# Kernel optimization log

Hardware: AMD Instinct MI355X
Metric: run time of the kernel (lower is better)

The kernel has to match this reference:

```python
import jax, jax.numpy as jnp
import numpy as np

NUM_EMBEDDINGS = 512
EMBEDDING_DIM = 64
COMMITMENT_COST = 0.25


def setup_inputs() -> dict:
    key = jax.random.key(0)
    k1, k2 = jax.random.split(key)
    inputs = jax.random.normal(k1, (64, 32, 32, EMBEDDING_DIM), dtype=jnp.float32)
    # nn.Embedding weight init: uniform(-1/K, 1/K)
    codebook = jax.random.uniform(
        k2, (NUM_EMBEDDINGS, EMBEDDING_DIM), dtype=jnp.float32,
        minval=-1.0 / NUM_EMBEDDINGS, maxval=1.0 / NUM_EMBEDDINGS)
    return {"inputs": inputs, "codebook": codebook}


def reference(inputs, codebook):
    D = codebook.shape[1]
    K = codebook.shape[0]
    flat = inputs.reshape(-1, D)  # [N, D]
    # Squared euclidean distances (argmin-equivalent to torch.cdist output)
    d2 = (jnp.sum(flat * flat, axis=1, keepdims=True)
          - 2.0 * (flat @ codebook.T)
          + jnp.sum(codebook * codebook, axis=1))  # [N, K]
    idx = jnp.argmin(d2, axis=1)  # [N]
    # Gather codebook rows (== one-hot @ codebook in the original)
    quantized = codebook[idx].reshape(inputs.shape)
    e_latent_loss = jnp.mean((jax.lax.stop_gradient(quantized) - inputs) ** 2)
    q_latent_loss = jnp.mean((quantized - jax.lax.stop_gradient(inputs)) ** 2)
    loss = q_latent_loss + COMMITMENT_COST * e_latent_loss
    # Straight-through estimator
    quantized_st = inputs + jax.lax.stop_gradient(quantized - inputs)
    # Perplexity from code usage histogram (== mean of one-hot encodings)
    n = flat.shape[0]
    avg_probs = jnp.zeros((K,), dtype=jnp.float32).at[idx].add(1.0) / n
    perplexity = jnp.exp(-jnp.sum(avg_probs * jnp.log(avg_probs + 1e-10)))
    encoding_indices = idx[:, None]  # [N, 1] to match torch unsqueeze(1)
    return (loss, quantized_st, perplexity, encoding_indices)
```

## Files before the change

kernel.cpp:

```cpp
#include <hip/hip_runtime.h>
#include <math.h>

#define K_EMB 512
#define DIM 64
#define NVEC 65536
#define OUT_LOSS 0
#define OUT_Q 1
#define OUT_PERP (1 + NVEC * DIM)
#define OUT_IDX (1 + NVEC * DIM + 1)
#define EPS2 1e-4f
#define FIX_CAP 16

typedef __attribute__((ext_vector_type(8))) short short8;
typedef __attribute__((ext_vector_type(4))) float float4v;


__device__ __forceinline__ unsigned short bf16_rn(float f) {
    unsigned u = __float_as_uint(f);
    return (unsigned short)((u + 0x7FFFu + ((u >> 16) & 1u)) >> 16);
}

__device__ __forceinline__ float np_pairwise8_sq(const float* v) {
    float r[8];
#pragma unroll
    for (int j = 0; j < 8; ++j) r[j] = __fmul_rn(v[j], v[j]);
#pragma unroll
    for (int i = 8; i < 64; i += 8) {
#pragma unroll
        for (int j = 0; j < 8; ++j) r[j] = __fadd_rn(r[j], __fmul_rn(v[i + j], v[i + j]));
    }
    return __fadd_rn(__fadd_rn(__fadd_rn(r[0], r[1]), __fadd_rn(r[2], r[3])),
                     __fadd_rn(__fadd_rn(r[4], r[5]), __fadd_rn(r[6], r[7])));
}

__global__ void vq_frag(const float* __restrict__ codebook, float* __restrict__ csq,
                        unsigned short* __restrict__ ahi, unsigned short* __restrict__ alo,
                        float4* __restrict__ csqf, unsigned* __restrict__ hist,
                        double* __restrict__ sse64) {
    const int tid = threadIdx.x;
    if (blockIdx.x < 16) {
        const int id = blockIdx.x * 256 + tid;
        const int t = id >> 7, step = (id >> 6) & 1, lane = id & 63;
        const int m = t * 16 + (lane & 15);
        const int kb = step * 32 + (lane >> 4) * 8;
        const float4* src = (const float4*)(codebook + (m << 6) + kb);
        float4 f0 = src[0], f1 = src[1];
        const float fs[8] = {f0.x, f0.y, f0.z, f0.w, f1.x, f1.y, f1.z, f1.w};
        short8 h, l;
#pragma unroll
        for (int j = 0; j < 8; ++j) {
            unsigned short hv = bf16_rn(fs[j]);
            float lof = fs[j] - __uint_as_float(((unsigned)hv) << 16);
            h[j] = (short)hv;
            l[j] = (short)bf16_rn(lof);
        }
        const int fo = ((t * 2 + step) * 64 + lane) * 8;
        *(short8*)(ahi + fo) = h;
        *(short8*)(alo + fo) = l;
    } else {
        __shared__ float s_csq[512];
#pragma unroll
        for (int r = 0; r < 2; ++r) {
            const int k = tid + 256 * r;
            float v = np_pairwise8_sq(codebook + ((size_t)k << 6));
            s_csq[k] = v;
            csq[k] = v;
            hist[k] = 0u;
        }
        if (tid < 64) sse64[tid] = 0.0;
        __syncthreads();
#pragma unroll
        for (int i = 0; i < 8; ++i) {
            const int id = i * 256 + tid;
            const int t = id >> 6, lane = id & 63;
            const int k0 = t * 16 + (lane >> 4) * 4;
            csqf[id] = make_float4(s_csq[k0], s_csq[k0 + 1], s_csq[k0 + 2], s_csq[k0 + 3]);
        }
    }
}

__launch_bounds__(256, 4)
__global__ void vq_main(const float* __restrict__ inputs, const float* __restrict__ codebook,
                        const float* __restrict__ csq, const unsigned short* __restrict__ ahi,
                        const unsigned short* __restrict__ alo, const float4* __restrict__ csqf,
                        unsigned* __restrict__ hist, double* __restrict__ sse64,
                        float* __restrict__ out) {
    __shared__ __align__(16) float s_x[32 * 68];
    __shared__ float s_A[32];
    __shared__ unsigned long long s_t1[4][32];
    __shared__ unsigned long long s_t2[4][32];
    __shared__ unsigned long long s_e[32];
    __shared__ int s_fix[FIX_CAP];
    __shared__ int s_nfix;
    __shared__ float s_w[4];

    const int tid = threadIdx.x;
    const int wave = tid >> 6, lane = tid & 63;
    const int vbase = blockIdx.x * 32;

    if (tid == 0) s_nfix = 0;

    {
        const float4* src = (const float4*)(inputs + ((size_t)vbase << 6));
#pragma unroll
        for (int i = 0; i < 2; ++i) {
            const int f = i * 256 + tid;
            float4 v = src[f];
            *(float4*)&s_x[(f >> 4) * 68 + (f & 15) * 4] = v;
        }
    }
    __syncthreads();

    if (tid < 32) s_A[tid] = np_pairwise8_sq(&s_x[tid * 68]);
    __syncthreads();

    short8 bhi[2][2], blo[2][2];
#pragma unroll
    for (int vt = 0; vt < 2; ++vt) {
        const int vrow = vt * 16 + (lane & 15);
#pragma unroll
        for (int step = 0; step < 2; ++step) {
            const int kb = step * 32 + (lane >> 4) * 8;
            float4 f0 = *(const float4*)&s_x[vrow * 68 + kb];
            float4 f1 = *(const float4*)&s_x[vrow * 68 + kb + 4];
            const float fs[8] = {f0.x, f0.y, f0.z, f0.w, f1.x, f1.y, f1.z, f1.w};
            short8 h, l;
#pragma unroll
            for (int j = 0; j < 8; ++j) {
                unsigned short hv = bf16_rn(fs[j]);
                float lof = fs[j] - __uint_as_float(((unsigned)hv) << 16);
                h[j] = (short)hv;
                l[j] = (short)bf16_rn(lof);
            }
            bhi[vt][step] = h;
            blo[vt][step] = l;
        }
    }

    unsigned long long e1[2] = {~0ULL, ~0ULL}, e2[2] = {~0ULL, ~0ULL};

#pragma unroll 2
    for (int tt = 0; tt < 8; ++tt) {
        const int t = wave * 8 + tt;
        const int fo0 = ((t * 2 + 0) * 64 + lane) * 8;
        const int fo1 = ((t * 2 + 1) * 64 + lane) * 8;
        short8 ah0 = *(const short8*)(ahi + fo0);
        short8 ah1 = *(const short8*)(ahi + fo1);
        short8 al0 = *(const short8*)(alo + fo0);
        short8 al1 = *(const short8*)(alo + fo1);
        float4 cs = csqf[t * 64 + lane];
        const float csr[4] = {cs.x, cs.y, cs.z, cs.w};
#pragma unroll
        for (int vt = 0; vt < 2; ++vt) {
            float4v acc = {0.f, 0.f, 0.f, 0.f};
            acc = __builtin_amdgcn_mfma_f32_16x16x32_bf16(ah0, bhi[vt][0], acc, 0, 0, 0);
            acc = __builtin_amdgcn_mfma_f32_16x16x32_bf16(ah1, bhi[vt][1], acc, 0, 0, 0);
            acc = __builtin_amdgcn_mfma_f32_16x16x32_bf16(ah0, blo[vt][0], acc, 0, 0, 0);
            acc = __builtin_amdgcn_mfma_f32_16x16x32_bf16(ah1, blo[vt][1], acc, 0, 0, 0);
            acc = __builtin_amdgcn_mfma_f32_16x16x32_bf16(al0, bhi[vt][0], acc, 0, 0, 0);
            acc = __builtin_amdgcn_mfma_f32_16x16x32_bf16(al1, bhi[vt][1], acc, 0, 0, 0);
            const float Avt = s_A[vt * 16 + (lane & 15)];
#pragma unroll
            for (int r = 0; r < 4; ++r) {
                float d2 = __fadd_rn(__fsub_rn(Avt, __fmul_rn(2.0f, acc[r])), csr[r]);
                const unsigned k = (unsigned)(t * 16 + (lane >> 4) * 4 + r);
                unsigned long long e = ((unsigned long long)__float_as_uint(d2) << 32) | k;
                if (e < e1[vt]) { e2[vt] = e1[vt]; e1[vt] = e; }
                else if (e < e2[vt]) e2[vt] = e;
            }
        }
    }

#pragma unroll
    for (int vt = 0; vt < 2; ++vt) {
#pragma unroll
        for (int off = 16; off <= 32; off <<= 1) {
            unsigned long long o1 = __shfl_xor(e1[vt], off);
            unsigned long long o2 = __shfl_xor(e2[vt], off);
            if (o1 < e1[vt]) { e2[vt] = (e1[vt] < o2) ? e1[vt] : o2; e1[vt] = o1; }
            else if (o1 < e2[vt]) e2[vt] = o1;
        }
        if (lane < 16) {
            s_t1[wave][vt * 16 + lane] = e1[vt];
            s_t2[wave][vt * 16 + lane] = e2[vt];
        }
    }
    __syncthreads();

    if (tid < 32) {
        unsigned long long E1 = ~0ULL, E2 = ~0ULL;
#pragma unroll
        for (int w = 0; w < 4; ++w) {
            unsigned long long a = s_t1[w][tid], b = s_t2[w][tid];
            if (a < E1) { E2 = (E1 < b) ? E1 : b; E1 = a; }
            else if (a < E2) E2 = a;
        }
        s_e[tid] = E1;
        float b1 = __uint_as_float((unsigned)(E1 >> 32));
        float b2 = __uint_as_float((unsigned)(E2 >> 32));
        if (__fsub_rn(b2, b1) <= EPS2) {
            int pos = atomicAdd(&s_nfix, 1);
            if (pos < FIX_CAP) s_fix[pos] = tid;
        }
    }
    __syncthreads();

    {
        int nf = s_nfix; if (nf > FIX_CAP) nf = FIX_CAP;
        for (int f = wave; f < nf; f += 4) {
            const int vloc = s_fix[f];
            const float* xr = &s_x[vloc * 68];
            const float A = s_A[vloc];
            unsigned long long best = ~0ULL;
#pragma unroll 1
            for (int r8 = 0; r8 < 8; ++r8) {
                const int k = lane * 8 + r8;
                const float* c = codebook + (k << 6);
                float p[8] = {0.f, 0.f, 0.f, 0.f, 0.f, 0.f, 0.f, 0.f};
#pragma unroll
                for (int ii = 0; ii < 64; ii += 8)
#pragma unroll
                    for (int j = 0; j < 8; ++j)
                        p[j] = __builtin_fmaf(xr[ii + j], c[ii + j], p[j]);
                float dot = __fadd_rn(__fadd_rn(__fadd_rn(p[0], p[1]), __fadd_rn(p[2], p[3])),
                                      __fadd_rn(__fadd_rn(p[4], p[5]), __fadd_rn(p[6], p[7])));
                float d2 = __fadd_rn(__fsub_rn(A, __fmul_rn(2.0f, dot)), csq[k]);
                unsigned long long e = ((unsigned long long)__float_as_uint(d2) << 32) | (unsigned)k;
                if (e < best) best = e;
            }
#pragma unroll
            for (int off = 32; off > 0; off >>= 1) {
                unsigned long long o = __shfl_down(best, off);
                if (o < best) best = o;
            }
            if (lane == 0) s_e[vloc] = best;
        }
    }
    __syncthreads();

    if (tid < 32) {
        const unsigned kf = (unsigned)s_e[tid];
        out[OUT_IDX + vbase + tid] = (float)kf;
        atomicAdd(&hist[kf], 1u);
    }
    {
        float4* dst = (float4*)(out + OUT_Q + ((size_t)vbase << 6));
        float es = 0.f;
#pragma unroll
        for (int i = 0; i < 2; ++i) {
            const int f = i * 256 + tid;
            const int row = f >> 4, col = (f & 15) * 4;
            const unsigned k = (unsigned)s_e[row];
            float4 qv = *(const float4*)(codebook + ((size_t)k << 6) + col);
            dst[f] = qv;
            float4 xv = *(const float4*)&s_x[row * 68 + col];
            float d0 = qv.x - xv.x; es = __builtin_fmaf(d0, d0, es);
            float d1 = qv.y - xv.y; es = __builtin_fmaf(d1, d1, es);
            float d2 = qv.z - xv.z; es = __builtin_fmaf(d2, d2, es);
            float d3 = qv.w - xv.w; es = __builtin_fmaf(d3, d3, es);
        }
#pragma unroll
        for (int off = 32; off > 0; off >>= 1) es += __shfl_down(es, off);
        if (lane == 0) s_w[wave] = es;
    }
    __syncthreads();
    if (tid == 0)
        atomicAdd(&sse64[blockIdx.x & 63],
                  (double)(((s_w[0] + s_w[1]) + (s_w[2] + s_w[3]))));
}

__global__ void vq_final(const unsigned* __restrict__ hist, const double* __restrict__ sse64,
                         float* __restrict__ out) {
    __shared__ float s_wsm[8];
    const int k = threadIdx.x;
    float pr = (float)hist[k] / 65536.0f;
    float v = __fmul_rn(pr, logf(__fadd_rn(pr, 1e-10f)));
#pragma unroll
    for (int off = 32; off > 0; off >>= 1) v += __shfl_down(v, off);
    if ((k & 63) == 0) s_wsm[k >> 6] = v;
    __syncthreads();
    if (k == 0) {
        float S = 0.f;
#pragma unroll
        for (int i = 0; i < 8; ++i) S += s_wsm[i];
        out[OUT_PERP] = expf(-S);
        double sv = 0.0;
        for (int i = 0; i < 64; ++i) sv += sse64[i];
        float m = (float)(sv / 4194304.0);
        out[OUT_LOSS] = __fadd_rn(m, __fmul_rn(0.25f, m));
    }
}

extern "C" void kernel_launch(void* const* d_in, const int* in_sizes, int n_in,
                              void* d_out, int out_size, void* d_ws, size_t ws_size,
                              hipStream_t stream) {
    const float* inputs   = (const float*)d_in[0];
    const float* codebook = (const float*)d_in[1];
    float* out = (float*)d_out;
    float*          csq   = (float*)d_ws;
    double*         sse64 = (double*)((char*)d_ws + 2048);
    unsigned*       hist  = (unsigned*)((char*)d_ws + 2560);
    unsigned short* ahi   = (unsigned short*)((char*)d_ws + 4608);
    unsigned short* alo   = (unsigned short*)((char*)d_ws + 70144);
    float4*         csqf  = (float4*)((char*)d_ws + 135680);

    vq_frag<<<17, 256, 0, stream>>>(codebook, csq, ahi, alo, csqf, hist, sse64);
    vq_main<<<2048, 256, 0, stream>>>(inputs, codebook, csq, ahi, alo, csqf, hist, sse64, out);
    vq_final<<<1, 512, 0, stream>>>(hist, sse64, out);
}
```

Measured before the change: 137.2 us.

## Fuse codebook prep into main kernel with LDS-resident fragments and persistent groups

Removes the separate codebook-prep kernel. Each 1024-thread block now splits the whole codebook into bf16 hi/lo MFMA fragments in LDS, along with the codebook squared norms, then loops over 4 groups of 32 input vectors. The goal is to drop one launch and the global-memory fragment loads, and to zero the workspace with a memset. The cost is that every block redoes the codebook conversion and holds roughly 140KB of LDS, which limits it to one block per CU. Each group is short and separated by block-wide barriers, which may cut latency hiding compared with the earlier four blocks per CU.

```diff
diff --git a/kernel.cpp b/kernel.cpp
--- a/kernel.cpp
+++ b/kernel.cpp
@@ -1,15 +1,15 @@
 #include <hip/hip_runtime.h>
 #include <math.h>
 
-#define K_EMB 512
-#define DIM 64
 #define NVEC 65536
 #define OUT_LOSS 0
 #define OUT_Q 1
-#define OUT_PERP (1 + NVEC * DIM)
-#define OUT_IDX (1 + NVEC * DIM + 1)
+#define OUT_PERP (1 + NVEC * 64)
+#define OUT_IDX (1 + NVEC * 64 + 1)
 #define EPS2 1e-4f
 #define FIX_CAP 16
+#define NBLK 512
+#define GRP 4
 
 typedef __attribute__((ext_vector_type(8))) short short8;
 typedef __attribute__((ext_vector_type(4))) float float4v;
@@ -33,96 +33,33 @@
                      __fadd_rn(__fadd_rn(r[4], r[5]), __fadd_rn(r[6], r[7])));
 }
 
-__global__ void vq_frag(const float* __restrict__ codebook, float* __restrict__ csq,
-                        unsigned short* __restrict__ ahi, unsigned short* __restrict__ alo,
-                        float4* __restrict__ csqf, unsigned* __restrict__ hist,
-                        double* __restrict__ sse64) {
-    const int tid = threadIdx.x;
-    if (blockIdx.x < 16) {
-        const int id = blockIdx.x * 256 + tid;
-        const int t = id >> 7, step = (id >> 6) & 1, lane = id & 63;
-        const int m = t * 16 + (lane & 15);
-        const int kb = step * 32 + (lane >> 4) * 8;
-        const float4* src = (const float4*)(codebook + (m << 6) + kb);
-        float4 f0 = src[0], f1 = src[1];
-        const float fs[8] = {f0.x, f0.y, f0.z, f0.w, f1.x, f1.y, f1.z, f1.w};
-        short8 h, l;
-#pragma unroll
-        for (int j = 0; j < 8; ++j) {
-            unsigned short hv = bf16_rn(fs[j]);
-            float lof = fs[j] - __uint_as_float(((unsigned)hv) << 16);
-            h[j] = (short)hv;
-            l[j] = (short)bf16_rn(lof);
-        }
-        const int fo = ((t * 2 + step) * 64 + lane) * 8;
-        *(short8*)(ahi + fo) = h;
-        *(short8*)(alo + fo) = l;
-    } else {
-        __shared__ float s_csq[512];
-#pragma unroll
-        for (int r = 0; r < 2; ++r) {
-            const int k = tid + 256 * r;
-            float v = np_pairwise8_sq(codebook + ((size_t)k << 6));
-            s_csq[k] = v;
-            csq[k] = v;
-            hist[k] = 0u;
-        }
-        if (tid < 64) sse64[tid] = 0.0;
-        __syncthreads();
-#pragma unroll
-        for (int i = 0; i < 8; ++i) {
-            const int id = i * 256 + tid;
-            const int t = id >> 6, lane = id & 63;
-            const int k0 = t * 16 + (lane >> 4) * 4;
-            csqf[id] = make_float4(s_csq[k0], s_csq[k0 + 1], s_csq[k0 + 2], s_csq[k0 + 3]);
-        }
-    }
-}
-
-__launch_bounds__(256, 4)
+__launch_bounds__(1024, 4)
 __global__ void vq_main(const float* __restrict__ inputs, const float* __restrict__ codebook,
-                        const float* __restrict__ csq, const unsigned short* __restrict__ ahi,
-                        const unsigned short* __restrict__ alo, const float4* __restrict__ csqf,
                         unsigned* __restrict__ hist, double* __restrict__ sse64,
                         float* __restrict__ out) {
-    __shared__ __align__(16) float s_x[32 * 68];
+    __shared__ short s_fhi[4096 * 8];
+    __shared__ short s_flo[4096 * 8];
+    __shared__ float s_csq[512];
+    __shared__ short s_bh[256 * 8];
+    __shared__ short s_bl[256 * 8];
     __shared__ float s_A[32];
-    __shared__ unsigned long long s_t1[4][32];
-    __shared__ unsigned long long s_t2[4][32];
+    __shared__ unsigned long long s_t1[16][32];
+    __shared__ unsigned long long s_t2[16][32];
     __shared__ unsigned long long s_e[32];
     __shared__ int s_fix[FIX_CAP];
     __shared__ int s_nfix;
-    __shared__ float s_w[4];
+    __shared__ float s_w[16];
 
     const int tid = threadIdx.x;
     const int wave = tid >> 6, lane = tid & 63;
-    const int vbase = blockIdx.x * 32;
-
-    if (tid == 0) s_nfix = 0;
 
     {
-        const float4* src = (const float4*)(inputs + ((size_t)vbase << 6));
-#pragma unroll
-        for (int i = 0; i < 2; ++i) {
-            const int f = i * 256 + tid;
-            float4 v = src[f];
-            *(float4*)&s_x[(f >> 4) * 68 + (f & 15) * 4] = v;
-        }
-    }
-    __syncthreads();
-
-    if (tid < 32) s_A[tid] = np_pairwise8_sq(&s_x[tid * 68]);
-    __syncthreads();
-
-    short8 bhi[2][2], blo[2][2];
-#pragma unroll
-    for (int vt = 0; vt < 2; ++vt) {
-        const int vrow = vt * 16 + (lane & 15);
-#pragma unroll
-        for (int step = 0; step < 2; ++step) {
-            const int kb = step * 32 + (lane >> 4) * 8;
-            float4 f0 = *(const float4*)&s_x[vrow * 68 + kb];
-            float4 f1 = *(const float4*)&s_x[vrow * 68 + kb + 4];
+        const float4* cb4 = (const float4*)codebook;
+#pragma unroll
+        for (int c = 0; c < 4; ++c) {
+            const int chunk = tid * 4 + c;
+            const int row = chunk >> 3, col8 = chunk & 7;
+            float4 f0 = cb4[chunk * 2 + 0], f1 = cb4[chunk * 2 + 1];
             const float fs[8] = {f0.x, f0.y, f0.z, f0.w, f1.x, f1.y, f1.z, f1.w};
             short8 h, l;
 #pragma unroll
@@ -132,141 +69,186 @@
                 h[j] = (short)hv;
                 l[j] = (short)bf16_rn(lof);
             }
-            bhi[vt][step] = h;
-            blo[vt][step] = l;
-        }
-    }
-
-    unsigned long long e1[2] = {~0ULL, ~0ULL}, e2[2] = {~0ULL, ~0ULL};
-
-#pragma unroll 2
-    for (int tt = 0; tt < 8; ++tt) {
-        const int t = wave * 8 + tt;
-        const int fo0 = ((t * 2 + 0) * 64 + lane) * 8;
-        const int fo1 = ((t * 2 + 1) * 64 + lane) * 8;
-        short8 ah0 = *(const short8*)(ahi + fo0);
-        short8 ah1 = *(const short8*)(ahi + fo1);
-        short8 al0 = *(const short8*)(alo + fo0);
-        short8 al1 = *(const short8*)(alo + fo1);
-        float4 cs = csqf[t * 64 + lane];
-        const float csr[4] = {cs.x, cs.y, cs.z, cs.w};
+            const int t = row >> 4;
+            const int ls = (row & 15) | ((col8 & 3) << 4);
+            const int st = col8 >> 2;
+            const int off = ((t * 2 + st) * 64 + ls) * 8;
+            *(short8*)&s_fhi[off] = h;
+            *(short8*)&s_flo[off] = l;
+        }
+        if (tid < 512) s_csq[tid] = np_pairwise8_sq(codebook + ((size_t)tid << 6));
+    }
+
+    float es = 0.f;
+
+#pragma unroll 1
+    for (int g = 0; g < GRP; ++g) {
+        const int vbase = (blockIdx.x * GRP + g) * 32;
+
+        if (tid < 256) {
+            const int vt = tid >> 7, st = (tid >> 6) & 1, ln = tid & 63;
+            const int vrow = vt * 16 + (ln & 15);
+            const int kb = st * 32 + (ln >> 4) * 8;
+            const float4* xp = (const float4*)(inputs + ((size_t)(vbase + vrow) << 6) + kb);
+            float4 f0 = xp[0], f1 = xp[1];
+            const float fs[8] = {f0.x, f0.y, f0.z, f0.w, f1.x, f1.y, f1.z, f1.w};
+            short8 h, l;
+#pragma unroll
+            for (int j = 0; j < 8; ++j) {
+                unsigned short hv = bf16_rn(fs[j]);
+                float lof = fs[j] - __uint_as_float(((unsigned)hv) << 16);
+                h[j] = (short)hv;
+                l[j] = (short)bf16_rn(lof);
+            }
+            const int off = ((vt * 2 + st) * 64 + ln) * 8;
+            *(short8*)&s_bh[off] = h;
+            *(short8*)&s_bl[off] = l;
+        } else if (tid < 288) {
+            s_A[tid - 256] = np_pairwise8_sq(inputs + ((size_t)(vbase + tid - 256) << 6));
+        } else if (tid == 288) {
+            s_nfix = 0;
+        }
+        __syncthreads();
+
+        short8 bh[2][2], bl[2][2];
+#pragma unroll
+        for (int vt = 0; vt < 2; ++vt)
+#pragma unroll
+            for (int st = 0; st < 2; ++st) {
+                const int off = ((vt * 2 + st) * 64 + lane) * 8;
+                bh[vt][st] = *(const short8*)&s_bh[off];
+                bl[vt][st] = *(const short8*)&s_bl[off];
+            }
+        const float Av[2] = {s_A[lane & 15], s_A[16 + (lane & 15)]};
+
+        unsigned long long e1[2] = {~0ULL, ~0ULL}, e2[2] = {~0ULL, ~0ULL};
+
+#pragma unroll
+        for (int tt = 0; tt < 2; ++tt) {
+            const int t = wave * 2 + tt;
+            const int fo = (t * 128 + lane) * 8;
+            short8 ah0 = *(const short8*)&s_fhi[fo];
+            short8 ah1 = *(const short8*)&s_fhi[fo + 512];
+            short8 al0 = *(const short8*)&s_flo[fo];
+            short8 al1 = *(const short8*)&s_flo[fo + 512];
+            const int k0 = t * 16 + (lane >> 4) * 4;
+            float4 cs = *(const float4*)&s_csq[k0];
+            const float csr[4] = {cs.x, cs.y, cs.z, cs.w};
+#pragma unroll
+            for (int vt = 0; vt < 2; ++vt) {
+                float4v a1 = {0.f, 0.f, 0.f, 0.f}, a2 = {0.f, 0.f, 0.f, 0.f};
+                a1 = __builtin_amdgcn_mfma_f32_16x16x32_bf16(ah0, bh[vt][0], a1, 0, 0, 0);
+                a1 = __builtin_amdgcn_mfma_f32_16x16x32_bf16(ah1, bh[vt][1], a1, 0, 0, 0);
+                a2 = __builtin_amdgcn_mfma_f32_16x16x32_bf16(ah0, bl[vt][0], a2, 0, 0, 0);
+                a2 = __builtin_amdgcn_mfma_f32_16x16x32_bf16(ah1, bl[vt][1], a2, 0, 0, 0);
+                a2 = __builtin_amdgcn_mfma_f32_16x16x32_bf16(al0, bh[vt][0], a2, 0, 0, 0);
+                a2 = __builtin_amdgcn_mfma_f32_16x16x32_bf16(al1, bh[vt][1], a2, 0, 0, 0);
+#pragma unroll
+                for (int r = 0; r < 4; ++r) {
+                    float dot = __fadd_rn(a1[r], a2[r]);
+                    float d2 = __fadd_rn(__fsub_rn(Av[vt], __fmul_rn(2.0f, dot)), csr[r]);
+                    const unsigned k = (unsigned)(k0 + r);
+                    unsigned long long e = ((unsigned long long)__float_as_uint(d2) << 32) | k;
+                    if (e < e1[vt]) { e2[vt] = e1[vt]; e1[vt] = e; }
+                    else if (e < e2[vt]) e2[vt] = e;
+                }
+            }
+        }
+
 #pragma unroll
         for (int vt = 0; vt < 2; ++vt) {
-            float4v acc = {0.f, 0.f, 0.f, 0.f};
-            acc = __builtin_amdgcn_mfma_f32_16x16x32_bf16(ah0, bhi[vt][0], acc, 0, 0, 0);
-            acc = __builtin_amdgcn_mfma_f32_16x16x32_bf16(ah1, bhi[vt][1], acc, 0, 0, 0);
-            acc = __builtin_amdgcn_mfma_f32_16x16x32_bf16(ah0, blo[vt][0], acc, 0, 0, 0);
-            acc = __builtin_amdgcn_mfma_f32_16x16x32_bf16(ah1, blo[vt][1], acc, 0, 0, 0);
-            acc = __builtin_amdgcn_mfma_f32_16x16x32_bf16(al0, bhi[vt][0], acc, 0, 0, 0);
-            acc = __builtin_amdgcn_mfma_f32_16x16x32_bf16(al1, bhi[vt][1], acc, 0, 0, 0);
-            const float Avt = s_A[vt * 16 + (lane & 15)];
-#pragma unroll
-            for (int r = 0; r < 4; ++r) {
-                float d2 = __fadd_rn(__fsub_rn(Avt, __fmul_rn(2.0f, acc[r])), csr[r]);
-                const unsigned k = (unsigned)(t * 16 + (lane >> 4) * 4 + r);
-                unsigned long long e = ((unsigned long long)__float_as_uint(d2) << 32) | k;
-                if (e < e1[vt]) { e2[vt] = e1[vt]; e1[vt] = e; }
-                else if (e < e2[vt]) e2[vt] = e;
-            }
-        }
-    }
-
-#pragma unroll
-    for (int vt = 0; vt < 2; ++vt) {
-#pragma unroll
-        for (int off = 16; off <= 32; off <<= 1) {
-            unsigned long long o1 = __shfl_xor(e1[vt], off);
-            unsigned long long o2 = __shfl_xor(e2[vt], off);
-            if (o1 < e1[vt]) { e2[vt] = (e1[vt] < o2) ? e1[vt] : o2; e1[vt] = o1; }
-            else if (o1 < e2[vt]) e2[vt] = o1;
-        }
-        if (lane < 16) {
-            s_t1[wave][vt * 16 + lane] = e1[vt];
-            s_t2[wave][vt * 16 + lane] = e2[vt];
-        }
-    }
-    __syncthreads();
-
-    if (tid < 32) {
-        unsigned long long E1 = ~0ULL, E2 = ~0ULL;
-#pragma unroll
-        for (int w = 0; w < 4; ++w) {
-            unsigned long long a = s_t1[w][tid], b = s_t2[w][tid];
-            if (a < E1) { E2 = (E1 < b) ? E1 : b; E1 = a; }
-            else if (a < E2) E2 = a;
-        }
-        s_e[tid] = E1;
-        float b1 = __uint_as_float((unsigned)(E1 >> 32));
-        float b2 = __uint_as_float((unsigned)(E2 >> 32));
-        if (__fsub_rn(b2, b1) <= EPS2) {
-            int pos = atomicAdd(&s_nfix, 1);
-            if (pos < FIX_CAP) s_fix[pos] = tid;
-        }
-    }
-    __syncthreads();
-
-    {
-        int nf = s_nfix; if (nf > FIX_CAP) nf = FIX_CAP;
-        for (int f = wave; f < nf; f += 4) {
-            const int vloc = s_fix[f];
-            const float* xr = &s_x[vloc * 68];
-            const float A = s_A[vloc];
-            unsigned long long best = ~0ULL;
+#pragma unroll
+            for (int off = 16; off <= 32; off <<= 1) {
+                unsigned long long o1 = __shfl_xor(e1[vt], off);
+                unsigned long long o2 = __shfl_xor(e2[vt], off);
+                if (o1 < e1[vt]) { e2[vt] = (e1[vt] < o2) ? e1[vt] : o2; e1[vt] = o1; }
+                else if (o1 < e2[vt]) e2[vt] = o1;
+            }
+            if (lane < 16) {
+                s_t1[wave][vt * 16 + lane] = e1[vt];
+                s_t2[wave][vt * 16 + lane] = e2[vt];
+            }
+        }
+        __syncthreads();
+
+        if (tid < 32) {
+            unsigned long long E1 = ~0ULL, E2 = ~0ULL;
+#pragma unroll
+            for (int w = 0; w < 16; ++w) {
+                unsigned long long a = s_t1[w][tid], b = s_t2[w][tid];
+                if (a < E1) { E2 = (E1 < b) ? E1 : b; E1 = a; }
+                else if (a < E2) E2 = a;
+            }
+            s_e[tid] = E1;
+            float b1 = __uint_as_float((unsigned)(E1 >> 32));
+            float b2 = __uint_as_float((unsigned)(E2 >> 32));
+            if (__fsub_rn(b2, b1) <= EPS2) {
+                int pos = atomicAdd(&s_nfix, 1);
+                if (pos < FIX_CAP) s_fix[pos] = tid;
+            }
+        }
+        __syncthreads();
+
+        {
+            int nf = s_nfix; if (nf > FIX_CAP) nf = FIX_CAP;
+            for (int f = wave; f < nf; f += 16) {
+                const int vloc = s_fix[f];
+                const float* xr = inputs + ((size_t)(vbase + vloc) << 6);
+                const float A = s_A[vloc];
+                unsigned long long best = ~0ULL;
 #pragma unroll 1
-            for (int r8 = 0; r8 < 8; ++r8) {
-                const int k = lane * 8 + r8;
-                const float* c = codebook + (k << 6);
-                float p[8] = {0.f, 0.f, 0.f, 0.f, 0.f, 0.f, 0.f, 0.f};
-#pragma unroll
-                for (int ii = 0; ii < 64; ii += 8)
-#pragma unroll
-                    for (int j = 0; j < 8; ++j)
-                        p[j] = __builtin_fmaf(xr[ii + j], c[ii + j], p[j]);
-                float dot = __fadd_rn(__fadd_rn(__fadd_rn(p[0], p[1]), __fadd_rn(p[2], p[3])),
-                                      __fadd_rn(__fadd_rn(p[4], p[5]), __fadd_rn(p[6], p[7])));
-                float d2 = __fadd_rn(__fsub_rn(A, __fmul_rn(2.0f, dot)), csq[k]);
-                unsigned long long e = ((unsigned long long)__float_as_uint(d2) << 32) | (unsigned)k;
-                if (e < best) best = e;
-            }
-#pragma unroll
-            for (int off = 32; off > 0; off >>= 1) {
-                unsigned long long o = __shfl_down(best, off);
-                if (o < best) best = o;
-            }
-            if (lane == 0) s_e[vloc] = best;
-        }
-    }
-    __syncthreads();
-
-    if (tid < 32) {
-        const unsigned kf = (unsigned)s_e[tid];
-        out[OUT_IDX + vbase + tid] = (float)kf;
-        atomicAdd(&hist[kf], 1u);
-    }
-    {
-        float4* dst = (float4*)(out + OUT_Q + ((size_t)vbase << 6));
-        float es = 0.f;
-#pragma unroll
-        for (int i = 0; i < 2; ++i) {
-            const int f = i * 256 + tid;
-            const int row = f >> 4, col = (f & 15) * 4;
+                for (int r8 = 0; r8 < 8; ++r8) {
+                    const int k = lane * 8 + r8;
+                    const float* c = codebook + (k << 6);
+                    float p[8] = {0.f, 0.f, 0.f, 0.f, 0.f, 0.f, 0.f, 0.f};
+#pragma unroll
+                    for (int ii = 0; ii < 64; ii += 8)
+#pragma unroll
+                        for (int j = 0; j < 8; ++j)
+                            p[j] = __builtin_fmaf(xr[ii + j], c[ii + j], p[j]);
+                    float dot = __fadd_rn(__fadd_rn(__fadd_rn(p[0], p[1]), __fadd_rn(p[2], p[3])),
+                                          __fadd_rn(__fadd_rn(p[4], p[5]), __fadd_rn(p[6], p[7])));
+                    float d2 = __fadd_rn(__fsub_rn(A, __fmul_rn(2.0f, dot)), s_csq[k]);
+                    unsigned long long e =
+                        ((unsigned long long)__float_as_uint(d2) << 32) | (unsigned)k;
+                    if (e < best) best = e;
+                }
+#pragma unroll
+                for (int off = 32; off > 0; off >>= 1) {
+                    unsigned long long o = __shfl_down(best, off);
+                    if (o < best) best = o;
+                }
+                if (lane == 0) s_e[vloc] = best;
+            }
+        }
+        __syncthreads();
+
+        if (tid < 32) {
+            const unsigned kf = (unsigned)s_e[tid];
+            out[OUT_IDX + vbase + tid] = (float)kf;
+            atomicAdd(&hist[kf], 1u);
+        }
+        {
+            const int row = tid >> 5, c2 = (tid & 31) * 2;
             const unsigned k = (unsigned)s_e[row];
-            float4 qv = *(const float4*)(codebook + ((size_t)k << 6) + col);
-            dst[f] = qv;
-            float4 xv = *(const float4*)&s_x[row * 68 + col];
+            const float2 qv = *(const float2*)(codebook + ((size_t)k << 6) + c2);
+            *(float2*)(out + OUT_Q + ((size_t)(vbase + row) << 6) + c2) = qv;
+            const float2 xv = *(const float2*)(inputs + ((size_t)(vbase + row) << 6) + c2);
             float d0 = qv.x - xv.x; es = __builtin_fmaf(d0, d0, es);
             float d1 = qv.y - xv.y; es = __builtin_fmaf(d1, d1, es);
-            float d2 = qv.z - xv.z; es = __builtin_fmaf(d2, d2, es);
-            float d3 = qv.w - xv.w; es = __builtin_fmaf(d3, d3, es);
-        }
-#pragma unroll
-        for (int off = 32; off > 0; off >>= 1) es += __shfl_down(es, off);
-        if (lane == 0) s_w[wave] = es;
-    }
+        }
+    }
+
+#pragma unroll
+    for (int off = 32; off > 0; off >>= 1) es += __shfl_down(es, off);
+    if (lane == 0) s_w[wave] = es;
     __syncthreads();
-    if (tid == 0)
-        atomicAdd(&sse64[blockIdx.x & 63],
-                  (double)(((s_w[0] + s_w[1]) + (s_w[2] + s_w[3]))));
+    if (tid == 0) {
+        float S = 0.f;
+#pragma unroll
+        for (int i = 0; i < 16; ++i) S += s_w[i];
+        atomicAdd(&sse64[blockIdx.x & 63], (double)S);
+    }
 }
 
 __global__ void vq_final(const unsigned* __restrict__ hist, const double* __restrict__ sse64,
@@ -297,14 +279,10 @@
     const float* inputs   = (const float*)d_in[0];
     const float* codebook = (const float*)d_in[1];
     float* out = (float*)d_out;
-    float*          csq   = (float*)d_ws;
-    double*         sse64 = (double*)((char*)d_ws + 2048);
-    unsigned*       hist  = (unsigned*)((char*)d_ws + 2560);
-    unsigned short* ahi   = (unsigned short*)((char*)d_ws + 4608);
-    unsigned short* alo   = (unsigned short*)((char*)d_ws + 70144);
-    float4*         csqf  = (float4*)((char*)d_ws + 135680);
-
-    vq_frag<<<17, 256, 0, stream>>>(codebook, csq, ahi, alo, csqf, hist, sse64);
-    vq_main<<<2048, 256, 0, stream>>>(inputs, codebook, csq, ahi, alo, csqf, hist, sse64, out);
+    double*   sse64 = (double*)d_ws;
+    unsigned* hist  = (unsigned*)((char*)d_ws + 512);
+
+    hipMemsetAsync(d_ws, 0, 2560, stream);
+    vq_main<<<NBLK, 1024, 0, stream>>>(inputs, codebook, hist, sse64, out);
     vq_final<<<1, 512, 0, stream>>>(hist, sse64, out);
 }
```

Result: slower. 203.1 us (+48.1%).
